# Kernel optimization log

Measured on AMD Instinct MI355X. Metric: run time of the kernel, lower is better.

## Reference

```python
import jax, jax.numpy as jnp
import numpy as np

Q = 128          # number of slices
S = 1024 // Q    # slice length = 8
U = 32           # hidden units per slice
EPS = 1e-3       # keras LayerNormalization default epsilon


def setup_inputs() -> dict:
    key = jax.random.key(0)
    ks = jax.random.split(key, 8)
    B = 16384
    x = jax.random.normal(ks[0], (B, 1, 1, Q * S), dtype=jnp.float32)
    # per-slice Dense1 (S->U), LayerNorm(gamma,beta), Dense2 (U->1)
    W1 = jax.random.normal(ks[1], (Q, S, U), dtype=jnp.float32) / np.sqrt(S)
    b1 = jnp.zeros((Q, U), dtype=jnp.float32)
    gamma = jnp.ones((Q, U), dtype=jnp.float32)
    beta = jnp.zeros((Q, U), dtype=jnp.float32)
    W2 = jax.random.normal(ks[2], (Q, U), dtype=jnp.float32) / np.sqrt(U)
    b2 = jnp.zeros((Q,), dtype=jnp.float32)
    return {"x": x, "W1": W1, "b1": b1, "gamma": gamma, "beta": beta,
            "W2": W2, "b2": b2}


def reference(x, W1, b1, gamma, beta, W2, b2):
    B = x.shape[0]
    xs = x.reshape(B, Q, S)                              # (B,Q,S)
    # batched tiny Dense -> ELU
    h = jnp.einsum('bqs,qsu->bqu', xs, W1) + b1          # (B,Q,U)
    h = jax.nn.elu(h)
    # per-slice LayerNorm over last axis
    mu = jnp.mean(h, axis=-1, keepdims=True)
    var = jnp.mean(jnp.square(h - mu), axis=-1, keepdims=True)
    h = (h - mu) * jax.lax.rsqrt(var + EPS) * gamma + beta
    # batched output projection U -> 1, concat over slices
    out = jnp.einsum('bqu,qu->bq', h, W2) + b2           # (B,Q)
    return out
```

## Files before the change

### kernel.cpp

```cpp
#include <hip/hip_runtime.h>


typedef __attribute__((ext_vector_type(8))) short short8;
typedef __attribute__((ext_vector_type(16))) float f32x16;

#define XS_STRIDE 40

__device__ __forceinline__ short fbits(__bf16 b) { return __builtin_bit_cast(short, b); }

__device__ __forceinline__ float elu1(float v) {
    return v > 0.f ? v : __expf(v) - 1.f;
}

__device__ __forceinline__ short4 cvt4(float4 v) {
    short4 r;
    r.x = fbits((__bf16)v.x); r.y = fbits((__bf16)v.y);
    r.z = fbits((__bf16)v.z); r.w = fbits((__bf16)v.w);
    return r;
}

__device__ __forceinline__ float finish(const f32x16& acc, const f32x16& g2r,
                                        float G, float C) {
    float sum = 0.f, ss = 0.f, dot = 0.f;
    #pragma unroll
    for (int r = 0; r < 16; ++r) {
        float e = elu1(acc[r]);
        sum += e;
        ss  = fmaf(e, e, ss);
        dot = fmaf(e, g2r[r], dot);
    }
    sum += __shfl_xor(sum, 32);
    ss  += __shfl_xor(ss, 32);
    dot += __shfl_xor(dot, 32);
    float mu  = sum * 0.03125f;
    float var = fmaf(-mu, mu, ss * 0.03125f);
    float inv = rsqrtf(var + 1e-3f);
    return fmaf(inv, fmaf(-mu, G, dot), C);
}

__global__ __launch_bounds__(256, 4) void divenc_mfma(
    const float* __restrict__ x,
    const float* __restrict__ W1,
    const float* __restrict__ b1,
    const float* __restrict__ gamma,
    const float* __restrict__ beta,
    const float* __restrict__ W2,
    const float* __restrict__ b2,
    float* __restrict__ out)
{
    __shared__ short xs[2][64 * XS_STRIDE];
    __shared__ float lout[256 * 5];

    const int tid  = threadIdx.x;
    const int w    = tid >> 6;
    const int ln   = tid & 63;
    const int u    = ln & 31;
    const int half = ln >> 5;
    const int qt   = blockIdx.y;
    const int q    = qt * 4 + w;
    const int bx   = blockIdx.x;
    const int band = bx * 256;

    const int srow0 = tid >> 3;
    const int srow1 = srow0 + 32;
    const int schk  = tid & 7;
    const float* xpan = x + qt * 32 + schk * 4;

    short8 wfrag;
    #pragma unroll
    for (int j = 0; j < 8; ++j) {
        float f  = W1[q * 256 + j * 32 + u];
        __bf16 h = (__bf16)f;
        wfrag[j] = half ? fbits((__bf16)(f - (float)h)) : fbits(h);
    }

    f32x16 biasr, g2r;
    float G, C;
    {
        float gs = 0.f, cs = 0.f;
        #pragma unroll
        for (int c = 0; c < 4; ++c) {
            const int ub = q * 32 + 4 * half + 8 * c;
            float4 b1v = *(const float4*)&b1[ub];
            float4 gav = *(const float4*)&gamma[ub];
            float4 w2v = *(const float4*)&W2[ub];
            float4 bev = *(const float4*)&beta[ub];
            #pragma unroll
            for (int j = 0; j < 4; ++j) {
                float g2 = ((const float*)&gav)[j] * ((const float*)&w2v)[j];
                biasr[4 * c + j] = ((const float*)&b1v)[j];
                g2r[4 * c + j]   = g2;
                gs += g2;
                cs += ((const float*)&bev)[j] * ((const float*)&w2v)[j];
            }
        }
        gs += __shfl_xor(gs, 32);
        cs += __shfl_xor(cs, 32);
        G = gs;
        C = cs + b2[q];
    }

    {
        float4 g0 = *(const float4*)(xpan + (size_t)(band + srow0) * 1024);
        float4 g1 = *(const float4*)(xpan + (size_t)(band + srow1) * 1024);
        *(short4*)&xs[0][srow0 * XS_STRIDE + schk * 4] = cvt4(g0);
        *(short4*)&xs[0][srow1 * XS_STRIDE + schk * 4] = cvt4(g1);
    }
    __syncthreads();

    #pragma unroll 1
    for (int it = 0; it < 4; ++it) {
        const int cur = it & 1;
        const int b0  = it * 64;

        float4 g0, g1;
        if (it < 3) {
            g0 = *(const float4*)(xpan + (size_t)(band + b0 + 64 + srow0) * 1024);
            g1 = *(const float4*)(xpan + (size_t)(band + b0 + 64 + srow1) * 1024);
        }

        short8 xa = *(const short8*)&xs[cur][u * XS_STRIDE + w * 8];
        short8 xb = *(const short8*)&xs[cur][(u + 32) * XS_STRIDE + w * 8];

        f32x16 acc0 = __builtin_amdgcn_mfma_f32_32x32x16_bf16(wfrag, xa, biasr, 0, 0, 0);
        f32x16 acc1 = __builtin_amdgcn_mfma_f32_32x32x16_bf16(wfrag, xb, biasr, 0, 0, 0);

        float res0 = finish(acc0, g2r, G, C);
        float res1 = finish(acc1, g2r, G, C);

        if (half == 0) {
            lout[(b0 + u) * 5 + w]      = res0;
            lout[(b0 + 32 + u) * 5 + w] = res1;
        }

        if (it < 3) {
            *(short4*)&xs[cur ^ 1][srow0 * XS_STRIDE + schk * 4] = cvt4(g0);
            *(short4*)&xs[cur ^ 1][srow1 * XS_STRIDE + schk * 4] = cvt4(g1);
        }
        __syncthreads();
    }

    {
        float4 o;
        o.x = lout[tid * 5 + 0];
        o.y = lout[tid * 5 + 1];
        o.z = lout[tid * 5 + 2];
        o.w = lout[tid * 5 + 3];
        *(float4*)(out + (size_t)(band + tid) * 128 + qt * 4) = o;
    }
}

extern "C" void kernel_launch(void* const* d_in, const int* in_sizes, int n_in,
                              void* d_out, int out_size, void* d_ws, size_t ws_size,
                              hipStream_t stream) {
    const float* x     = (const float*)d_in[0];
    const float* W1    = (const float*)d_in[1];
    const float* b1    = (const float*)d_in[2];
    const float* gamma = (const float*)d_in[3];
    const float* beta  = (const float*)d_in[4];
    const float* W2    = (const float*)d_in[5];
    const float* b2    = (const float*)d_in[6];
    float* out = (float*)d_out;

    dim3 grid(64, 32);
    divenc_mfma<<<grid, 256, 0, stream>>>(x, W1, b1, gamma, beta, W2, b2, out);
}
```

Baseline: 28.66 us.

## Give each wave private LDS panel covering all four slices, drop block barriers

Work is reassigned so that each wave owns 32 batch rows and computes all four slices of the block's slice group, instead of one slice per wave across 64 shared rows. Each wave stages its rows in a private LDS panel, which removes every __syncthreads and the shared output staging buffer. Results are now written straight to global memory as float4 per row. Each block covers 512 rows, so the grid is halved, and each thread keeps four sets of weight fragments and constants, which raises register use. Launch bounds are lowered to 2 blocks per CU to allow that, at the cost of occupancy.

```diff
diff --git a/kernel.cpp b/kernel.cpp
--- a/kernel.cpp
+++ b/kernel.cpp
@@ -4,7 +4,7 @@
 typedef __attribute__((ext_vector_type(8))) short short8;
 typedef __attribute__((ext_vector_type(16))) float f32x16;
 
-#define XS_STRIDE 40
+#define PITCH 40
 
 __device__ __forceinline__ short fbits(__bf16 b) { return __builtin_bit_cast(short, b); }
 
@@ -19,26 +19,7 @@
     return r;
 }
 
-__device__ __forceinline__ float finish(const f32x16& acc, const f32x16& g2r,
-                                        float G, float C) {
-    float sum = 0.f, ss = 0.f, dot = 0.f;
-    #pragma unroll
-    for (int r = 0; r < 16; ++r) {
-        float e = elu1(acc[r]);
-        sum += e;
-        ss  = fmaf(e, e, ss);
-        dot = fmaf(e, g2r[r], dot);
-    }
-    sum += __shfl_xor(sum, 32);
-    ss  += __shfl_xor(ss, 32);
-    dot += __shfl_xor(dot, 32);
-    float mu  = sum * 0.03125f;
-    float var = fmaf(-mu, mu, ss * 0.03125f);
-    float inv = rsqrtf(var + 1e-3f);
-    return fmaf(inv, fmaf(-mu, G, dot), C);
-}
-
-__global__ __launch_bounds__(256, 4) void divenc_mfma(
+__global__ __launch_bounds__(256, 2) void divenc_mfma(
     const float* __restrict__ x,
     const float* __restrict__ W1,
     const float* __restrict__ b1,
@@ -48,8 +29,7 @@
     const float* __restrict__ b2,
     float* __restrict__ out)
 {
-    __shared__ short xs[2][64 * XS_STRIDE];
-    __shared__ float lout[256 * 5];
+    __shared__ short xs[4][32 * PITCH];
 
     const int tid  = threadIdx.x;
     const int w    = tid >> 6;
@@ -57,26 +37,31 @@
     const int u    = ln & 31;
     const int half = ln >> 5;
     const int qt   = blockIdx.y;
-    const int q    = qt * 4 + w;
     const int bx   = blockIdx.x;
-    const int band = bx * 256;
+    const int band = bx * 512;
+    short* panel   = &xs[w][0];
 
-    const int srow0 = tid >> 3;
-    const int srow1 = srow0 + 32;
-    const int schk  = tid & 7;
-    const float* xpan = x + qt * 32 + schk * 4;
+    const int srow = ln >> 3;
+    const int schk = ln & 7;
+    const float* xg = x + qt * 32 + schk * 4;
 
-    short8 wfrag;
+    short8 wfrag[4];
     #pragma unroll
-    for (int j = 0; j < 8; ++j) {
-        float f  = W1[q * 256 + j * 32 + u];
-        __bf16 h = (__bf16)f;
-        wfrag[j] = half ? fbits((__bf16)(f - (float)h)) : fbits(h);
+    for (int qq = 0; qq < 4; ++qq) {
+        const int q = qt * 4 + qq;
+        #pragma unroll
+        for (int j = 0; j < 8; ++j) {
+            float f  = W1[q * 256 + j * 32 + u];
+            __bf16 h = (__bf16)f;
+            wfrag[qq][j] = half ? fbits((__bf16)(f - (float)h)) : fbits(h);
+        }
     }
 
-    f32x16 biasr, g2r;
-    float G, C;
-    {
+    f32x16 biasr[4], g2r[4];
+    float G[4], C[4];
+    #pragma unroll
+    for (int qq = 0; qq < 4; ++qq) {
+        const int q = qt * 4 + qq;
         float gs = 0.f, cs = 0.f;
         #pragma unroll
         for (int c = 0; c < 4; ++c) {
@@ -88,65 +73,78 @@
             #pragma unroll
             for (int j = 0; j < 4; ++j) {
                 float g2 = ((const float*)&gav)[j] * ((const float*)&w2v)[j];
-                biasr[4 * c + j] = ((const float*)&b1v)[j];
-                g2r[4 * c + j]   = g2;
+                biasr[qq][4 * c + j] = ((const float*)&b1v)[j];
+                g2r[qq][4 * c + j]   = g2;
                 gs += g2;
                 cs += ((const float*)&bev)[j] * ((const float*)&w2v)[j];
             }
         }
         gs += __shfl_xor(gs, 32);
         cs += __shfl_xor(cs, 32);
-        G = gs;
-        C = cs + b2[q];
+        G[qq] = gs;
+        C[qq] = cs + b2[q];
     }
 
     {
-        float4 g0 = *(const float4*)(xpan + (size_t)(band + srow0) * 1024);
-        float4 g1 = *(const float4*)(xpan + (size_t)(band + srow1) * 1024);
-        *(short4*)&xs[0][srow0 * XS_STRIDE + schk * 4] = cvt4(g0);
-        *(short4*)&xs[0][srow1 * XS_STRIDE + schk * 4] = cvt4(g1);
+        const float* base = xg + (size_t)(band + w * 32 + srow) * 1024;
+        float4 a0 = *(const float4*)(base);
+        float4 a1 = *(const float4*)(base +  8 * 1024);
+        float4 a2 = *(const float4*)(base + 16 * 1024);
+        float4 a3 = *(const float4*)(base + 24 * 1024);
+        *(short4*)&panel[(srow     ) * PITCH + schk * 4] = cvt4(a0);
+        *(short4*)&panel[(srow +  8) * PITCH + schk * 4] = cvt4(a1);
+        *(short4*)&panel[(srow + 16) * PITCH + schk * 4] = cvt4(a2);
+        *(short4*)&panel[(srow + 24) * PITCH + schk * 4] = cvt4(a3);
     }
-    __syncthreads();
 
     #pragma unroll 1
     for (int it = 0; it < 4; ++it) {
-        const int cur = it & 1;
-        const int b0  = it * 64;
+        const int rowbase = band + it * 128 + w * 32;
 
-        float4 g0, g1;
+        float4 n0, n1, n2, n3;
         if (it < 3) {
-            g0 = *(const float4*)(xpan + (size_t)(band + b0 + 64 + srow0) * 1024);
-            g1 = *(const float4*)(xpan + (size_t)(band + b0 + 64 + srow1) * 1024);
+            const float* nb = xg + (size_t)(rowbase + 128 + srow) * 1024;
+            n0 = *(const float4*)(nb);
+            n1 = *(const float4*)(nb +  8 * 1024);
+            n2 = *(const float4*)(nb + 16 * 1024);
+            n3 = *(const float4*)(nb + 24 * 1024);
         }
 
-        short8 xa = *(const short8*)&xs[cur][u * XS_STRIDE + w * 8];
-        short8 xb = *(const short8*)&xs[cur][(u + 32) * XS_STRIDE + w * 8];
+        float res[4];
+        #pragma unroll
+        for (int qq = 0; qq < 4; ++qq) {
+            short8 xf = *(const short8*)&panel[u * PITCH + qq * 8];
+            f32x16 acc = __builtin_amdgcn_mfma_f32_32x32x16_bf16(
+                             wfrag[qq], xf, biasr[qq], 0, 0, 0);
 
-        f32x16 acc0 = __builtin_amdgcn_mfma_f32_32x32x16_bf16(wfrag, xa, biasr, 0, 0, 0);
-        f32x16 acc1 = __builtin_amdgcn_mfma_f32_32x32x16_bf16(wfrag, xb, biasr, 0, 0, 0);
-
-        float res0 = finish(acc0, g2r, G, C);
-        float res1 = finish(acc1, g2r, G, C);
+            float sum = 0.f, ss = 0.f, dot = 0.f;
+            #pragma unroll
+            for (int r = 0; r < 16; ++r) {
+                float e = elu1(acc[r]);
+                sum += e;
+                ss  = fmaf(e, e, ss);
+                dot = fmaf(e, g2r[qq][r], dot);
+            }
+            sum += __shfl_xor(sum, 32);
+            ss  += __shfl_xor(ss, 32);
+            dot += __shfl_xor(dot, 32);
+            float mu  = sum * 0.03125f;
+            float var = fmaf(-mu, mu, ss * 0.03125f);
+            float inv = rsqrtf(var + 1e-3f);
+            res[qq] = fmaf(inv, fmaf(-mu, G[qq], dot), C[qq]);
+        }
 
         if (half == 0) {
-            lout[(b0 + u) * 5 + w]      = res0;
-            lout[(b0 + 32 + u) * 5 + w] = res1;
+            float4 o = {res[0], res[1], res[2], res[3]};
+            *(float4*)(out + (size_t)(rowbase + u) * 128 + qt * 4) = o;
         }
 
         if (it < 3) {
-            *(short4*)&xs[cur ^ 1][srow0 * XS_STRIDE + schk * 4] = cvt4(g0);
-            *(short4*)&xs[cur ^ 1][srow1 * XS_STRIDE + schk * 4] = cvt4(g1);
+            *(short4*)&panel[(srow     ) * PITCH + schk * 4] = cvt4(n0);
+            *(short4*)&panel[(srow +  8) * PITCH + schk * 4] = cvt4(n1);
+            *(short4*)&panel[(srow + 16) * PITCH + schk * 4] = cvt4(n2);
+            *(short4*)&panel[(srow + 24) * PITCH + schk * 4] = cvt4(n3);
         }
-        __syncthreads();
-    }
-
-    {
-        float4 o;
-        o.x = lout[tid * 5 + 0];
-        o.y = lout[tid * 5 + 1];
-        o.z = lout[tid * 5 + 2];
-        o.w = lout[tid * 5 + 3];
-        *(float4*)(out + (size_t)(band + tid) * 128 + qt * 4) = o;
     }
 }
 
@@ -162,6 +160,6 @@
     const float* b2    = (const float*)d_in[6];
     float* out = (float*)d_out;
 
-    dim3 grid(64, 32);
+    dim3 grid(32, 32);
     divenc_mfma<<<grid, 256, 0, stream>>>(x, W1, b1, gamma, beta, W2, b2, out);
 }
```

After: 43.25 us. 1.51x slower.

## Use 512-thread blocks with triple-buffered LDS and two-deep global prefetch

Applied to the files above, without the earlier changes.

Blocks grow to 8 waves, with each pair of waves splitting a slice's 64-row batch tile, so every wave issues one MFMA per iteration instead of two. Global loads are prefetched two tiles ahead into registers, staged through a three-slot LDS ring, and synchronized by a barrier that waits only on LDS counters, not on outstanding global loads. The intent is to keep more loads in flight and hide memory latency. The cost is fewer blocks, more iterations per block, and extra register and LDS use per block.

```diff
diff --git a/kernel.cpp b/kernel.cpp
--- a/kernel.cpp
+++ b/kernel.cpp
@@ -19,26 +19,12 @@
     return r;
 }
 
-__device__ __forceinline__ float finish(const f32x16& acc, const f32x16& g2r,
-                                        float G, float C) {
-    float sum = 0.f, ss = 0.f, dot = 0.f;
-    #pragma unroll
-    for (int r = 0; r < 16; ++r) {
-        float e = elu1(acc[r]);
-        sum += e;
-        ss  = fmaf(e, e, ss);
-        dot = fmaf(e, g2r[r], dot);
-    }
-    sum += __shfl_xor(sum, 32);
-    ss  += __shfl_xor(ss, 32);
-    dot += __shfl_xor(dot, 32);
-    float mu  = sum * 0.03125f;
-    float var = fmaf(-mu, mu, ss * 0.03125f);
-    float inv = rsqrtf(var + 1e-3f);
-    return fmaf(inv, fmaf(-mu, G, dot), C);
+__device__ __forceinline__ void barrier_ds_only() {
+    asm volatile("s_waitcnt lgkmcnt(0)" ::: "memory");
+    __builtin_amdgcn_s_barrier();
 }
 
-__global__ __launch_bounds__(256, 4) void divenc_mfma(
+__global__ __launch_bounds__(512, 8) void divenc_mfma8(
     const float* __restrict__ x,
     const float* __restrict__ W1,
     const float* __restrict__ b1,
@@ -48,22 +34,23 @@
     const float* __restrict__ b2,
     float* __restrict__ out)
 {
-    __shared__ short xs[2][64 * XS_STRIDE];
-    __shared__ float lout[256 * 5];
+    __shared__ short xs[3][64 * XS_STRIDE];
+    __shared__ float lout[512 * 5];
 
     const int tid  = threadIdx.x;
     const int w    = tid >> 6;
     const int ln   = tid & 63;
     const int u    = ln & 31;
     const int half = ln >> 5;
+    const int qq   = w >> 1;
+    const int th   = w & 1;
     const int qt   = blockIdx.y;
-    const int q    = qt * 4 + w;
+    const int q    = qt * 4 + qq;
     const int bx   = blockIdx.x;
-    const int band = bx * 256;
+    const int band = bx * 512;
 
-    const int srow0 = tid >> 3;
-    const int srow1 = srow0 + 32;
-    const int schk  = tid & 7;
+    const int srow = tid >> 3;
+    const int schk = tid & 7;
     const float* xpan = x + qt * 32 + schk * 4;
 
     short8 wfrag;
@@ -101,44 +88,54 @@
     }
 
     {
-        float4 g0 = *(const float4*)(xpan + (size_t)(band + srow0) * 1024);
-        float4 g1 = *(const float4*)(xpan + (size_t)(band + srow1) * 1024);
-        *(short4*)&xs[0][srow0 * XS_STRIDE + schk * 4] = cvt4(g0);
-        *(short4*)&xs[0][srow1 * XS_STRIDE + schk * 4] = cvt4(g1);
+        float4 g0 = *(const float4*)(xpan + (size_t)(band + srow) * 1024);
+        *(short4*)&xs[0][srow * XS_STRIDE + schk * 4] = cvt4(g0);
     }
-    __syncthreads();
+    float4 p0 = *(const float4*)(xpan + (size_t)(band + 64 + srow) * 1024);
+    barrier_ds_only();
 
     #pragma unroll 1
-    for (int it = 0; it < 4; ++it) {
-        const int cur = it & 1;
+    for (int it = 0; it < 8; ++it) {
+        const int cur = it % 3;
+        const int nxt = (it + 1) % 3;
         const int b0  = it * 64;
 
-        float4 g0, g1;
-        if (it < 3) {
-            g0 = *(const float4*)(xpan + (size_t)(band + b0 + 64 + srow0) * 1024);
-            g1 = *(const float4*)(xpan + (size_t)(band + b0 + 64 + srow1) * 1024);
+        float4 f0;
+        if (it < 6)
+            f0 = *(const float4*)(xpan + (size_t)(band + b0 + 128 + srow) * 1024);
+
+        short8 xa = *(const short8*)&xs[cur][(th * 32 + u) * XS_STRIDE + qq * 8];
+
+        f32x16 acc = __builtin_amdgcn_mfma_f32_32x32x16_bf16(wfrag, xa, biasr, 0, 0, 0);
+
+        {
+            float sum = 0.f, ss = 0.f, dot = 0.f;
+            #pragma unroll
+            for (int r = 0; r < 16; ++r) {
+                float e = elu1(acc[r]);
+                sum += e;
+                ss  = fmaf(e, e, ss);
+                dot = fmaf(e, g2r[r], dot);
+            }
+            sum += __shfl_xor(sum, 32);
+            ss  += __shfl_xor(ss, 32);
+            dot += __shfl_xor(dot, 32);
+            float mu  = sum * 0.03125f;
+            float var = fmaf(-mu, mu, ss * 0.03125f);
+            float inv = rsqrtf(var + 1e-3f);
+            float res = fmaf(inv, fmaf(-mu, G, dot), C);
+            if (half == 0) lout[(b0 + th * 32 + u) * 5 + qq] = res;
         }
 
-        short8 xa = *(const short8*)&xs[cur][u * XS_STRIDE + w * 8];
-        short8 xb = *(const short8*)&xs[cur][(u + 32) * XS_STRIDE + w * 8];
-
-        f32x16 acc0 = __builtin_amdgcn_mfma_f32_32x32x16_bf16(wfrag, xa, biasr, 0, 0, 0);
-        f32x16 acc1 = __builtin_amdgcn_mfma_f32_32x32x16_bf16(wfrag, xb, biasr, 0, 0, 0);
-
-        float res0 = finish(acc0, g2r, G, C);
-        float res1 = finish(acc1, g2r, G, C);
-
-        if (half == 0) {
-            lout[(b0 + u) * 5 + w]      = res0;
-            lout[(b0 + 32 + u) * 5 + w] = res1;
+        if (it < 7) {
+            *(short4*)&xs[nxt][srow * XS_STRIDE + schk * 4] = cvt4(p0);
+            barrier_ds_only();
         }
 
-        if (it < 3) {
-            *(short4*)&xs[cur ^ 1][srow0 * XS_STRIDE + schk * 4] = cvt4(g0);
-            *(short4*)&xs[cur ^ 1][srow1 * XS_STRIDE + schk * 4] = cvt4(g1);
-        }
-        __syncthreads();
+        p0 = f0;
     }
+
+    __syncthreads();
 
     {
         float4 o;
@@ -162,6 +159,6 @@
     const float* b2    = (const float*)d_in[6];
     float* out = (float*)d_out;
 
-    dim3 grid(64, 32);
-    divenc_mfma<<<grid, 256, 0, stream>>>(x, W1, b1, gamma, beta, W2, b2, out);
+    dim3 grid(32, 32);
+    divenc_mfma8<<<grid, 512, 0, stream>>>(x, W1, b1, gamma, beta, W2, b2, out);
 }
```

After: 39.59 us. 1.38x slower.
